# Performance work log

Hardware: AMD Instinct MI355X
Metric: run time of the kernel (lower is better)

Reference implementation:

```python
import jax, jax.numpy as jnp
import numpy as np

N = 50000
D_IN = 128
D_OUT = 128
EPS = 1e-5


def setup_inputs() -> dict:
    key = jax.random.key(0)
    ks = jax.random.split(key, 10)
    x = jax.random.normal(ks[0], (N, D_IN), dtype=jnp.float32)
    edge_index = jax.random.randint(ks[1], (2, 800000), 0, N, dtype=jnp.int64)
    s_in = 1.0 / np.sqrt(D_IN)
    s_out = 1.0 / np.sqrt(D_OUT)
    return {
        "x": x,
        "edge_index": edge_index,
        # SAGEConv 1: lin_l (on aggregated neighbors, with bias), lin_r (root, no bias)
        "w1_l": jax.random.uniform(ks[2], (D_OUT, D_IN), jnp.float32, -s_in, s_in),
        "b1_l": jnp.zeros((D_OUT,), jnp.float32),
        "w1_r": jax.random.uniform(ks[3], (D_OUT, D_IN), jnp.float32, -s_in, s_in),
        # SAGEConv 2
        "w2_l": jax.random.uniform(ks[4], (D_OUT, D_OUT), jnp.float32, -s_out, s_out),
        "b2_l": jnp.zeros((D_OUT,), jnp.float32),
        "w2_r": jax.random.uniform(ks[5], (D_OUT, D_OUT), jnp.float32, -s_out, s_out),
        # BatchNorm affine params
        "bn_gamma": jnp.ones((D_OUT,), jnp.float32),
        "bn_beta": jnp.zeros((D_OUT,), jnp.float32),
    }


def _sage_conv(x, src, dst, w_l, b_l, w_r):
    # mean aggregation of source-node features into target nodes
    msg = x[src]                                              # [E, D]
    agg = jax.ops.segment_sum(msg, dst, num_segments=N)       # [N, D]
    cnt = jax.ops.segment_sum(jnp.ones((src.shape[0],), x.dtype), dst, num_segments=N)
    mean = agg / jnp.maximum(cnt, 1.0)[:, None]
    return mean @ w_l.T + b_l + x @ w_r.T


def _batch_norm(x, gamma, beta):
    mu = jnp.mean(x, axis=0)
    var = jnp.mean(jnp.square(x - mu), axis=0)  # biased, as in torch BN training
    return (x - mu) * jax.lax.rsqrt(var + EPS) * gamma + beta


def reference(x, edge_index, w1_l, b1_l, w1_r, w2_l, b2_l, w2_r, bn_gamma, bn_beta):
    src, dst = edge_index[0], edge_index[1]
    h = _sage_conv(x, src, dst, w1_l, b1_l, w1_r)
    h = _batch_norm(h, bn_gamma, bn_beta)
    h = jax.nn.relu(h)
    out = _sage_conv(h, src, dst, w2_l, b2_l, w2_r)
    return out
```

## Files before the change

### kernel.cpp

```cpp
#include <hip/hip_runtime.h>

#define D 128
#define EPS 1e-5f
#define SCAN_CHUNK 2048
#define FB_EPB 8

typedef unsigned int uint;
typedef __attribute__((ext_vector_type(4))) float f32x4;
typedef __attribute__((ext_vector_type(8))) short s16x8;

__device__ __forceinline__ uint pack_bf16(float a, float b)
{
    uint ua = __float_as_uint(a);
    uint ub = __float_as_uint(b);
    ua += 0x7FFFu + ((ua >> 16) & 1u);
    ub += 0x7FFFu + ((ub >> 16) & 1u);
    return (ua >> 16) | (ub & 0xFFFF0000u);
}
__device__ __forceinline__ float bf_lo(uint v) { return __uint_as_float(v << 16); }
__device__ __forceinline__ float bf_hi(uint v) { return __uint_as_float(v & 0xFFFF0000u); }

__global__ void prep_kernel(const float* __restrict__ x, uint* __restrict__ xb, int ncvt,
                            const float* __restrict__ w1l, const float* __restrict__ w1r,
                            const float* __restrict__ w2l, const float* __restrict__ w2r,
                            uint* __restrict__ wb1, uint* __restrict__ wb2,
                            const int* __restrict__ dst, int* __restrict__ deg, int E)
{
    int idx = blockIdx.x * 256 + threadIdx.x;
    if (idx < ncvt) {
        float4 v = ((const float4*)x)[idx];
        uint2 o;
        o.x = pack_bf16(v.x, v.y);
        o.y = pack_bf16(v.z, v.w);
        ((uint2*)xb)[idx] = o;
    } else if (idx < ncvt + 8192) {
        int r = idx - ncvt;
        int layer = r >> 12;
        int rem = r & 4095;
        int lane = rem & 63;
        int knt = rem >> 6;
        int kstep = knt >> 3, nt = knt & 7;
        int nn = nt * 16 + (lane & 15);
        int kbase = kstep * 32 + (lane >> 4) * 8;
        const float* wl = layer ? w2l : w1l;
        const float* wr = layer ? w2r : w1r;
        uint* wb = layer ? wb2 : wb1;
        float v[8];
#pragma unroll
        for (int j = 0; j < 8; j++) {
            int k = kbase + j;
            v[j] = (k < D) ? wl[nn * D + k] : wr[nn * D + (k - D)];
        }
        uint4 o;
        o.x = pack_bf16(v[0], v[1]);
        o.y = pack_bf16(v[2], v[3]);
        o.z = pack_bf16(v[4], v[5]);
        o.w = pack_bf16(v[6], v[7]);
        ((uint4*)wb)[(kstep * 8 + nt) * 64 + lane] = o;
    } else {
        int e = idx - (ncvt + 8192);
        if (e < E) atomicAdd(&deg[dst[e]], 1);
    }
}

__global__ __launch_bounds__(256) void scanA_kernel(const int* __restrict__ deg,
                                                    int* __restrict__ bsum, int n)
{
    __shared__ int red[256];
    int base = blockIdx.x * SCAN_CHUNK;
    int s = 0;
    for (int i = threadIdx.x; i < SCAN_CHUNK; i += 256) {
        int idx = base + i;
        if (idx < n) s += deg[idx];
    }
    red[threadIdx.x] = s;
    __syncthreads();
    for (int off = 128; off > 0; off >>= 1) {
        if (threadIdx.x < off) red[threadIdx.x] += red[threadIdx.x + off];
        __syncthreads();
    }
    if (threadIdx.x == 0) bsum[blockIdx.x] = red[0];
}

__global__ void scanB_kernel(int* __restrict__ bsum, int nb)
{
    int t = threadIdx.x;
    int v = (t < nb) ? bsum[t] : 0;
    for (int off = 1; off < 64; off <<= 1) {
        int u = __shfl_up(v, off);
        if (t >= off) v += u;
    }
    int ex = __shfl_up(v, 1);
    if (t == 0) ex = 0;
    if (t < nb) bsum[t] = ex;
}

__global__ __launch_bounds__(256) void scanC_kernel(const int* __restrict__ deg,
                                                    const int* __restrict__ bsum,
                                                    int* __restrict__ rowptr,
                                                    int* __restrict__ bcur, int n, int E)
{
    __shared__ int tsum[256];
    int t = threadIdx.x;
    int tb = blockIdx.x * SCAN_CHUNK + t * 8;
    int v[8];
    int s = 0;
#pragma unroll
    for (int k = 0; k < 8; k++) {
        int idx = tb + k;
        v[k] = (idx < n) ? deg[idx] : 0;
        s += v[k];
    }
    tsum[t] = s;
    __syncthreads();
    for (int off = 1; off < 256; off <<= 1) {
        int u = (t >= off) ? tsum[t - off] : 0;
        __syncthreads();
        tsum[t] += u;
        __syncthreads();
    }
    int run = bsum[blockIdx.x] + tsum[t] - s;
#pragma unroll
    for (int k = 0; k < 8; k++) {
        int idx = tb + k;
        if (idx < n) {
            rowptr[idx] = run;
            if ((idx & 511) == 0) bcur[(idx >> 9) * 16] = run;
            run += v[k];
        }
    }
    if (blockIdx.x == 0 && t == 0) rowptr[n] = E;
}

__global__ __launch_bounds__(512) void bfill_kernel(const int* __restrict__ src,
                                                    const int* __restrict__ dst,
                                                    int* __restrict__ bcur,
                                                    uint2* __restrict__ ebuf,
                                                    int E, int nbuck)
{
    __shared__ int cnt[128], base[128];
    int t = threadIdx.x;
    if (t < 128) cnt[t] = 0;
    __syncthreads();
    int e0 = blockIdx.x * (512 * FB_EPB);
    int s[FB_EPB], d[FB_EPB], loc[FB_EPB];
#pragma unroll
    for (int k = 0; k < FB_EPB; k++) {
        int e = e0 + k * 512 + t;
        if (e < E) {
            s[k] = src[e];
            d[k] = dst[e];
            loc[k] = atomicAdd(&cnt[d[k] >> 9], 1);
        }
    }
    __syncthreads();
    if (t < nbuck) base[t] = atomicAdd(&bcur[t * 16], cnt[t]);
    __syncthreads();
#pragma unroll
    for (int k = 0; k < FB_EPB; k++) {
        int e = e0 + k * 512 + t;
        if (e < E) {
            int b = d[k] >> 9;
            ebuf[base[b] + loc[k]] = make_uint2((uint)s[k], (uint)d[k]);
        }
    }
}

__global__ __launch_bounds__(512) void pfill_kernel(const int* __restrict__ rowptr,
                                                    const uint2* __restrict__ ebuf,
                                                    int* __restrict__ col, int n)
{
    __shared__ int lcur[512];
    int t = threadIdx.x;
    int nb = blockIdx.x << 9;
    int ncnt = min(512, n - nb);
    if (t < ncnt) lcur[t] = rowptr[nb + t];
    __syncthreads();
    int e0 = rowptr[nb];
    int e1 = rowptr[min(nb + 512, n)];
    for (int i = e0 + t; i < e1; i += 512) {
        uint2 ed = ebuf[i];
        int p = atomicAdd(&lcur[(int)ed.y - nb], 1);
        col[p] = (int)ed.x;
    }
}

template<bool BN>
__global__ __launch_bounds__(256) void agg_kernel(const int* __restrict__ rowptr,
                                                  const int* __restrict__ col,
                                                  const uint* __restrict__ featb,
                                                  const float* __restrict__ scsh,
                                                  uint* __restrict__ aggb, int n)
{
    int node = blockIdx.x * 4 + (threadIdx.x >> 6);
    if (node >= n) return;
    int lane = threadIdx.x & 63;
    int sub = lane >> 4, l16 = lane & 15;
    int r0 = rowptr[node], r1 = rowptr[node + 1];
    uint4* out4 = (uint4*)aggb;
    if (r0 == r1) {
        if (lane < 16) out4[(size_t)node * 16 + l16] = make_uint4(0, 0, 0, 0);
        return;
    }
    float sc[8], sh[8];
    if (BN) {
        float4 s0 = ((const float4*)scsh)[l16 * 2];
        float4 s1 = ((const float4*)scsh)[l16 * 2 + 1];
        float4 t0 = ((const float4*)scsh)[32 + l16 * 2];
        float4 t1 = ((const float4*)scsh)[32 + l16 * 2 + 1];
        sc[0] = s0.x; sc[1] = s0.y; sc[2] = s0.z; sc[3] = s0.w;
        sc[4] = s1.x; sc[5] = s1.y; sc[6] = s1.z; sc[7] = s1.w;
        sh[0] = t0.x; sh[1] = t0.y; sh[2] = t0.z; sh[3] = t0.w;
        sh[4] = t1.x; sh[5] = t1.y; sh[6] = t1.z; sh[7] = t1.w;
    }
    float acc[8] = {0.f, 0.f, 0.f, 0.f, 0.f, 0.f, 0.f, 0.f};
    const uint4* fb = (const uint4*)featb;
    int last = r1 - 1;

    for (int i = r0; i < r1; i += 32) {
        uint4 v[8];
#pragma unroll
        for (int r = 0; r < 8; r++) {
            int idx = i + r * 4 + sub;
            int c = col[min(idx, last)];
            v[r] = fb[(size_t)c * 16 + l16];
        }
#pragma unroll
        for (int r = 0; r < 8; r++) {
            bool valid = (i + r * 4 + sub) < r1;
            uint4 u = v[r];
            float e[8] = {bf_lo(u.x), bf_hi(u.x), bf_lo(u.y), bf_hi(u.y),
                          bf_lo(u.z), bf_hi(u.z), bf_lo(u.w), bf_hi(u.w)};
#pragma unroll
            for (int j = 0; j < 8; j++) {
                float t = e[j];
                if (BN) t = fmaxf(t * sc[j] + sh[j], 0.f);
                acc[j] += valid ? t : 0.f;
            }
        }
    }
#pragma unroll
    for (int j = 0; j < 8; j++) {
        acc[j] += __shfl_down(acc[j], 32);
        acc[j] += __shfl_down(acc[j], 16);
    }
    if (lane < 16) {
        float inv = 1.0f / (float)(r1 - r0);
        uint4 o;
        o.x = pack_bf16(acc[0] * inv, acc[1] * inv);
        o.y = pack_bf16(acc[2] * inv, acc[3] * inv);
        o.z = pack_bf16(acc[4] * inv, acc[5] * inv);
        o.w = pack_bf16(acc[6] * inv, acc[7] * inv);
        out4[(size_t)node * 16 + l16] = o;
    }
}

#define TSTRIDE 132
template<bool FUSE1, bool BNP2>
__global__ __launch_bounds__(256) void conv_kernel(
    const uint* __restrict__ p1b, const uint* __restrict__ p2b,
    const uint* __restrict__ wb, const float* __restrict__ bias,
    const float* __restrict__ scsh, float* __restrict__ outf,
    uint* __restrict__ outb, float* __restrict__ pstats, int n)
{
    extern __shared__ float smem[];
    float* tile = smem;
    float* scs = smem;
    int w = threadIdx.x >> 6, lane = threadIdx.x & 63;
    int quad = lane >> 4, l15 = lane & 15;
    int nb = blockIdx.x * 64;

    if (BNP2) {
        scs[threadIdx.x] = scsh[threadIdx.x];
        __syncthreads();
    }

    const uint4* p1 = (const uint4*)p1b;
    const uint4* p2 = (const uint4*)p2b;
    const uint4* wv = (const uint4*)wb;

    uint4 B[8][2];
    int nt0 = w * 2;
#pragma unroll
    for (int ks = 0; ks < 8; ks++) {
#pragma unroll
        for (int t = 0; t < 2; t++)
            B[ks][t] = wv[(ks * 8 + nt0 + t) * 64 + lane];
    }

    float bv0 = bias[nt0 * 16 + l15];
    float bv1 = bias[nt0 * 16 + 16 + l15];

    for (int rt = 0; rt < 4; rt++) {
        int node = nb + rt * 16 + l15;
        int nc = min(node, n - 1);
        uint4 A[8];
#pragma unroll
        for (int ks = 0; ks < 4; ks++) A[ks] = p1[(size_t)nc * 16 + ks * 4 + quad];
#pragma unroll
        for (int ks = 0; ks < 4; ks++) A[ks + 4] = p2[(size_t)nc * 16 + ks * 4 + quad];

        if (BNP2) {
#pragma unroll
            for (int ks = 4; ks < 8; ks++) {
                int c0 = (ks - 4) * 32 + quad * 8;
                uint4 u = A[ks];
                float e[8] = {bf_lo(u.x), bf_hi(u.x), bf_lo(u.y), bf_hi(u.y),
                              bf_lo(u.z), bf_hi(u.z), bf_lo(u.w), bf_hi(u.w)};
#pragma unroll
                for (int j = 0; j < 8; j++)
                    e[j] = fmaxf(e[j] * scs[c0 + j] + scs[128 + c0 + j], 0.f);
                u.x = pack_bf16(e[0], e[1]);
                u.y = pack_bf16(e[2], e[3]);
                u.z = pack_bf16(e[4], e[5]);
                u.w = pack_bf16(e[6], e[7]);
                A[ks] = u;
            }
        }

        f32x4 acc0 = {bv0, bv0, bv0, bv0};
        f32x4 acc1 = {bv1, bv1, bv1, bv1};
#pragma unroll
        for (int ks = 0; ks < 8; ks++) {
            s16x8 a = *(s16x8*)&A[ks];
            acc0 = __builtin_amdgcn_mfma_f32_16x16x32_bf16(a, *(s16x8*)&B[ks][0], acc0, 0, 0, 0);
            acc1 = __builtin_amdgcn_mfma_f32_16x16x32_bf16(a, *(s16x8*)&B[ks][1], acc1, 0, 0, 0);
        }
        int row0 = nb + rt * 16 + quad * 4;
        int colbase = nt0 * 16 + l15;
        if (FUSE1) {
            int rloc0 = rt * 16 + quad * 4;
#pragma unroll
            for (int reg = 0; reg < 4; reg++) {
                bool ok = (row0 + reg) < n;
                tile[(rloc0 + reg) * TSTRIDE + colbase]      = ok ? acc0[reg] : 0.f;
                tile[(rloc0 + reg) * TSTRIDE + colbase + 16] = ok ? acc1[reg] : 0.f;
            }
        } else {
#pragma unroll
            for (int reg = 0; reg < 4; reg++) {
                int row = row0 + reg;
                if (row < n) {
                    outf[(size_t)row * D + colbase] = acc0[reg];
                    outf[(size_t)row * D + colbase + 16] = acc1[reg];
                }
            }
        }
    }

    if (FUSE1) {
        __syncthreads();
        int colj = threadIdx.x & 127, half = threadIdx.x >> 7;
        float s = 0.f, ss = 0.f;
        for (int r = half * 32; r < half * 32 + 32; r++) {
            float v = tile[r * TSTRIDE + colj];
            s += v;
            ss += v * v;
        }
        float* pb = pstats + (size_t)blockIdx.x * 512 + half * 256;
        pb[colj] = s;
        pb[128 + colj] = ss;
        uint4* ob4 = (uint4*)outb;
#pragma unroll
        for (int q4 = 0; q4 < 4; q4++) {
            int idx = q4 * 256 + threadIdx.x;
            int r = idx >> 4, q = idx & 15;
            int row = nb + r;
            if (row < n) {
                float* tr = &tile[r * TSTRIDE + q * 8];
                uint4 o;
                o.x = pack_bf16(tr[0], tr[1]);
                o.y = pack_bf16(tr[2], tr[3]);
                o.z = pack_bf16(tr[4], tr[5]);
                o.w = pack_bf16(tr[6], tr[7]);
                ob4[(size_t)row * 16 + q] = o;
            }
        }
    }
}

__global__ __launch_bounds__(256) void reduce_kernel(const float* __restrict__ pstats,
                                                     float* __restrict__ stats, int nparts)
{
    int j = threadIdx.x;
    int chunk = (nparts + gridDim.x - 1) / gridDim.x;
    int p0 = blockIdx.x * chunk;
    int p1 = min(p0 + chunk, nparts);
    float s = 0.f;
    for (int p = p0; p < p1; p++) s += pstats[(size_t)p * 256 + j];
    unsafeAtomicAdd(&stats[j], s);
}

__global__ void bnfin_kernel(const float* __restrict__ stats, const float* __restrict__ gamma,
                             const float* __restrict__ beta, float* __restrict__ scsh, float n_inv)
{
    int j = threadIdx.x;
    float mean = stats[j] * n_inv;
    float var = fmaxf(stats[128 + j] * n_inv - mean * mean, 0.f);
    float sc = gamma[j] * rsqrtf(var + EPS);
    scsh[j] = sc;
    scsh[128 + j] = beta[j] - mean * sc;
}

extern "C" void kernel_launch(void* const* d_in, const int* in_sizes, int n_in,
                              void* d_out, int out_size, void* d_ws, size_t ws_size,
                              hipStream_t stream)
{
    const float* x     = (const float*)d_in[0];
    const int*   ei    = (const int*)d_in[1];
    const float* w1_l  = (const float*)d_in[2];
    const float* b1_l  = (const float*)d_in[3];
    const float* w1_r  = (const float*)d_in[4];
    const float* w2_l  = (const float*)d_in[5];
    const float* b2_l  = (const float*)d_in[6];
    const float* w2_r  = (const float*)d_in[7];
    const float* gamma = (const float*)d_in[8];
    const float* beta  = (const float*)d_in[9];

    int N = in_sizes[0] / D;
    int E = in_sizes[1] / 2;
    const int* src = ei;
    const int* dst = ei + E;

    int cblocks = (N + 63) / 64;
    int nbuck   = (N + 511) >> 9;

    uint*  aggb   = (uint*)d_ws;
    uint*  xb     = aggb + (size_t)N * 64;
    uint*  hb     = xb + (size_t)N * 64;
    uint*  wb1    = hb + (size_t)N * 64;
    uint*  wb2    = wb1 + 16384;
    uint2* ebuf   = (uint2*)(wb2 + 16384);
    float* stats  = (float*)(ebuf + E);
    float* scsh   = stats + 256;
    float* pstats = scsh + 256;
    int*   deg    = (int*)(pstats + (size_t)cblocks * 512);
    int*   rowptr = deg + N;
    int*   col    = rowptr + N + 1;
    int*   bsum   = col + E;
    int*   bcur   = bsum + 64;

    hipMemsetAsync(deg, 0, (size_t)N * sizeof(int), stream);
    hipMemsetAsync(stats, 0, 256 * sizeof(float), stream);

    int ncvt = N * 32;
    int pblocks = (ncvt + 8192 + E + 255) / 256;
    prep_kernel<<<pblocks, 256, 0, stream>>>(x, xb, ncvt, w1_l, w1_r, w2_l, w2_r,
                                             wb1, wb2, dst, deg, E);

    int ablocks  = (N + 3) / 4;
    int bfblocks = (E + 4095) / 4096;
    int nscan    = (N + SCAN_CHUNK - 1) / SCAN_CHUNK;

    scanA_kernel<<<nscan, 256, 0, stream>>>(deg, bsum, N);
    scanB_kernel<<<1, 64, 0, stream>>>(bsum, nscan);
    scanC_kernel<<<nscan, 256, 0, stream>>>(deg, bsum, rowptr, bcur, N, E);
    bfill_kernel<<<bfblocks, 512, 0, stream>>>(src, dst, bcur, ebuf, E, nbuck);
    pfill_kernel<<<nbuck, 512, 0, stream>>>(rowptr, ebuf, col, N);

    agg_kernel<false><<<ablocks, 256, 0, stream>>>(rowptr, col, xb, nullptr, aggb, N);
    conv_kernel<true, false><<<cblocks, 256, 64 * TSTRIDE * 4, stream>>>(
        aggb, xb, wb1, b1_l, nullptr, nullptr, hb, pstats, N);

    reduce_kernel<<<32, 256, 0, stream>>>(pstats, stats, cblocks * 2);
    bnfin_kernel<<<1, 128, 0, stream>>>(stats, gamma, beta, scsh, 1.0f / (float)N);

    agg_kernel<true><<<ablocks, 256, 0, stream>>>(rowptr, col, hb, scsh, aggb, N);
    conv_kernel<false, true><<<cblocks, 256, 256 * 4, stream>>>(
        aggb, hb, wb2, b2_l, scsh, (float*)d_out, nullptr, nullptr, N);
}
```

Baseline: 291.1 us.

## Replace global degree atomics and node scan with bucket-count radix CSR build

```diff
diff --git a/kernel.cpp b/kernel.cpp
--- a/kernel.cpp
+++ b/kernel.cpp
@@ -2,7 +2,6 @@
 
 #define D 128
 #define EPS 1e-5f
-#define SCAN_CHUNK 2048
 #define FB_EPB 8
 
 typedef unsigned int uint;
@@ -23,8 +22,7 @@
 __global__ void prep_kernel(const float* __restrict__ x, uint* __restrict__ xb, int ncvt,
                             const float* __restrict__ w1l, const float* __restrict__ w1r,
                             const float* __restrict__ w2l, const float* __restrict__ w2r,
-                            uint* __restrict__ wb1, uint* __restrict__ wb2,
-                            const int* __restrict__ dst, int* __restrict__ deg, int E)
+                            uint* __restrict__ wb1, uint* __restrict__ wb2)
 {
     int idx = blockIdx.x * 256 + threadIdx.x;
     if (idx < ncvt) {
@@ -57,86 +55,55 @@
         o.z = pack_bf16(v[4], v[5]);
         o.w = pack_bf16(v[6], v[7]);
         ((uint4*)wb)[(kstep * 8 + nt) * 64 + lane] = o;
-    } else {
-        int e = idx - (ncvt + 8192);
-        if (e < E) atomicAdd(&deg[dst[e]], 1);
-    }
-}
-
-__global__ __launch_bounds__(256) void scanA_kernel(const int* __restrict__ deg,
-                                                    int* __restrict__ bsum, int n)
-{
-    __shared__ int red[256];
-    int base = blockIdx.x * SCAN_CHUNK;
+    }
+}
+
+__global__ __launch_bounds__(512) void bcount_kernel(const int* __restrict__ dst,
+                                                     int* __restrict__ bcnt,
+                                                     int E, int nblk, int nbuck)
+{
+    __shared__ int cnt[128];
+    int t = threadIdx.x;
+    if (t < 128) cnt[t] = 0;
+    __syncthreads();
+    int e0 = blockIdx.x * (512 * FB_EPB);
+#pragma unroll
+    for (int k = 0; k < FB_EPB; k++) {
+        int e = e0 + k * 512 + t;
+        if (e < E) atomicAdd(&cnt[dst[e] >> 9], 1);
+    }
+    __syncthreads();
+    if (t < nbuck) bcnt[t * nblk + blockIdx.x] = cnt[t];
+}
+
+__global__ __launch_bounds__(1024) void bscan_kernel(int* __restrict__ bcnt, int M)
+{
+    __shared__ int sums[1024];
+    int t = threadIdx.x;
+    int chunk = (M + 1023) / 1024;
+    int b0 = t * chunk;
+    int b1 = min(b0 + chunk, M);
+    int v[32];
     int s = 0;
-    for (int i = threadIdx.x; i < SCAN_CHUNK; i += 256) {
-        int idx = base + i;
-        if (idx < n) s += deg[idx];
-    }
-    red[threadIdx.x] = s;
-    __syncthreads();
-    for (int off = 128; off > 0; off >>= 1) {
-        if (threadIdx.x < off) red[threadIdx.x] += red[threadIdx.x + off];
-        __syncthreads();
-    }
-    if (threadIdx.x == 0) bsum[blockIdx.x] = red[0];
-}
-
-__global__ void scanB_kernel(int* __restrict__ bsum, int nb)
-{
-    int t = threadIdx.x;
-    int v = (t < nb) ? bsum[t] : 0;
-    for (int off = 1; off < 64; off <<= 1) {
-        int u = __shfl_up(v, off);
-        if (t >= off) v += u;
-    }
-    int ex = __shfl_up(v, 1);
-    if (t == 0) ex = 0;
-    if (t < nb) bsum[t] = ex;
-}
-
-__global__ __launch_bounds__(256) void scanC_kernel(const int* __restrict__ deg,
-                                                    const int* __restrict__ bsum,
-                                                    int* __restrict__ rowptr,
-                                                    int* __restrict__ bcur, int n, int E)
-{
-    __shared__ int tsum[256];
-    int t = threadIdx.x;
-    int tb = blockIdx.x * SCAN_CHUNK + t * 8;
-    int v[8];
-    int s = 0;
-#pragma unroll
-    for (int k = 0; k < 8; k++) {
-        int idx = tb + k;
-        v[k] = (idx < n) ? deg[idx] : 0;
-        s += v[k];
-    }
-    tsum[t] = s;
-    __syncthreads();
-    for (int off = 1; off < 256; off <<= 1) {
-        int u = (t >= off) ? tsum[t - off] : 0;
-        __syncthreads();
-        tsum[t] += u;
-        __syncthreads();
-    }
-    int run = bsum[blockIdx.x] + tsum[t] - s;
-#pragma unroll
-    for (int k = 0; k < 8; k++) {
-        int idx = tb + k;
-        if (idx < n) {
-            rowptr[idx] = run;
-            if ((idx & 511) == 0) bcur[(idx >> 9) * 16] = run;
-            run += v[k];
-        }
-    }
-    if (blockIdx.x == 0 && t == 0) rowptr[n] = E;
-}
-
-__global__ __launch_bounds__(512) void bfill_kernel(const int* __restrict__ src,
-                                                    const int* __restrict__ dst,
-                                                    int* __restrict__ bcur,
-                                                    uint2* __restrict__ ebuf,
-                                                    int E, int nbuck)
+    for (int i = b0; i < b1; i++) { v[i - b0] = bcnt[i]; s += v[i - b0]; }
+    sums[t] = s;
+    __syncthreads();
+    for (int off = 1; off < 1024; off <<= 1) {
+        int u = (t >= off) ? sums[t - off] : 0;
+        __syncthreads();
+        sums[t] += u;
+        __syncthreads();
+    }
+    int run = sums[t] - s;
+    for (int i = b0; i < b1; i++) { bcnt[i] = run; run += v[i - b0]; }
+    if (t == 1023) bcnt[M] = sums[1023];
+}
+
+__global__ __launch_bounds__(512) void bscatter_kernel(const int* __restrict__ src,
+                                                       const int* __restrict__ dst,
+                                                       const int* __restrict__ bcnt,
+                                                       uint2* __restrict__ ebuf,
+                                                       int E, int nblk, int nbuck)
 {
     __shared__ int cnt[128], base[128];
     int t = threadIdx.x;
@@ -154,7 +121,7 @@
         }
     }
     __syncthreads();
-    if (t < nbuck) base[t] = atomicAdd(&bcur[t * 16], cnt[t]);
+    if (t < nbuck) base[t] = bcnt[t * nblk + blockIdx.x];
     __syncthreads();
 #pragma unroll
     for (int k = 0; k < FB_EPB; k++) {
@@ -166,21 +133,41 @@
     }
 }
 
-__global__ __launch_bounds__(512) void pfill_kernel(const int* __restrict__ rowptr,
-                                                    const uint2* __restrict__ ebuf,
-                                                    int* __restrict__ col, int n)
-{
-    __shared__ int lcur[512];
+__global__ __launch_bounds__(512) void pbuild_kernel(const int* __restrict__ bcnt,
+                                                     const uint2* __restrict__ ebuf,
+                                                     int* __restrict__ rowptr,
+                                                     int* __restrict__ col,
+                                                     int n, int nblk, int nbuck, int M, int E)
+{
+    __shared__ int lcnt[512], lscan[512];
     int t = threadIdx.x;
-    int nb = blockIdx.x << 9;
+    int b = blockIdx.x;
+    int nb = b << 9;
+    int e0 = bcnt[b * nblk];
+    int e1 = (b + 1 < nbuck) ? bcnt[(b + 1) * nblk] : bcnt[M];
+    lcnt[t] = 0;
+    __syncthreads();
+    for (int i = e0 + t; i < e1; i += 512)
+        atomicAdd(&lcnt[(int)ebuf[i].y - nb], 1);
+    __syncthreads();
+    int s = lcnt[t];
+    lscan[t] = s;
+    __syncthreads();
+    for (int off = 1; off < 512; off <<= 1) {
+        int u = (t >= off) ? lscan[t - off] : 0;
+        __syncthreads();
+        lscan[t] += u;
+        __syncthreads();
+    }
+    int start = e0 + lscan[t] - s;
     int ncnt = min(512, n - nb);
-    if (t < ncnt) lcur[t] = rowptr[nb + t];
-    __syncthreads();
-    int e0 = rowptr[nb];
-    int e1 = rowptr[min(nb + 512, n)];
+    if (t < ncnt) rowptr[nb + t] = start;
+    if (b == nbuck - 1 && t == 0) rowptr[n] = E;
+    lscan[t] = start;
+    __syncthreads();
     for (int i = e0 + t; i < e1; i += 512) {
         uint2 ed = ebuf[i];
-        int p = atomicAdd(&lcur[(int)ed.y - nb], 1);
+        int p = atomicAdd(&lscan[(int)ed.y - nb], 1);
         col[p] = (int)ed.x;
     }
 }
@@ -424,6 +411,8 @@
 
     int cblocks = (N + 63) / 64;
     int nbuck   = (N + 511) >> 9;
+    int nblk    = (E + 4095) / 4096;
+    int M       = nbuck * nblk;
 
     uint*  aggb   = (uint*)d_ws;
     uint*  xb     = aggb + (size_t)N * 64;
@@ -434,29 +423,22 @@
     float* stats  = (float*)(ebuf + E);
     float* scsh   = stats + 256;
     float* pstats = scsh + 256;
-    int*   deg    = (int*)(pstats + (size_t)cblocks * 512);
-    int*   rowptr = deg + N;
+    int*   rowptr = (int*)(pstats + (size_t)cblocks * 512);
     int*   col    = rowptr + N + 1;
-    int*   bsum   = col + E;
-    int*   bcur   = bsum + 64;
-
-    hipMemsetAsync(deg, 0, (size_t)N * sizeof(int), stream);
+    int*   bcnt   = col + E;
+
     hipMemsetAsync(stats, 0, 256 * sizeof(float), stream);
 
     int ncvt = N * 32;
-    int pblocks = (ncvt + 8192 + E + 255) / 256;
-    prep_kernel<<<pblocks, 256, 0, stream>>>(x, xb, ncvt, w1_l, w1_r, w2_l, w2_r,
-                                             wb1, wb2, dst, deg, E);
-
-    int ablocks  = (N + 3) / 4;
-    int bfblocks = (E + 4095) / 4096;
-    int nscan    = (N + SCAN_CHUNK - 1) / SCAN_CHUNK;
-
-    scanA_kernel<<<nscan, 256, 0, stream>>>(deg, bsum, N);
-    scanB_kernel<<<1, 64, 0, stream>>>(bsum, nscan);
-    scanC_kernel<<<nscan, 256, 0, stream>>>(deg, bsum, rowptr, bcur, N, E);
-    bfill_kernel<<<bfblocks, 512, 0, stream>>>(src, dst, bcur, ebuf, E, nbuck);
-    pfill_kernel<<<nbuck, 512, 0, stream>>>(rowptr, ebuf, col, N);
+    int pblocks = (ncvt + 8192 + 255) / 256;
+    prep_kernel<<<pblocks, 256, 0, stream>>>(x, xb, ncvt, w1_l, w1_r, w2_l, w2_r, wb1, wb2);
+
+    int ablocks = (N + 3) / 4;
+
+    bcount_kernel<<<nblk, 512, 0, stream>>>(dst, bcnt, E, nblk, nbuck);
+    bscan_kernel<<<1, 1024, 0, stream>>>(bcnt, M);
+    bscatter_kernel<<<nblk, 512, 0, stream>>>(src, dst, bcnt, ebuf, E, nblk, nbuck);
+    pbuild_kernel<<<nbuck, 512, 0, stream>>>(bcnt, ebuf, rowptr, col, N, nblk, nbuck, M, E);
 
     agg_kernel<false><<<ablocks, 256, 0, stream>>>(rowptr, col, xb, nullptr, aggb, N);
     conv_kernel<true, false><<<cblocks, 256, 64 * TSTRIDE * 4, stream>>>(
```

New measurement: 265.2 us. -8.9%, faster.
